# Optimization experiments

Measured on AMD Instinct MI355X. Metric: run time of the kernel, lower is better.

The kernel has to match this reference:

```python
import jax, jax.numpy as jnp
import numpy as np

N = 50000          # nodes
E = 1600000        # edges
IN_C = 128
HID = 128
OUT_C = 1
NUM_LAYERS = 3     # extra conv2 applications
NUM_GRAPHS = 128


def setup_inputs() -> dict:
    key = jax.random.key(0)
    ks = jax.random.split(key, 10)
    x = jax.random.normal(ks[0], (N, IN_C), dtype=jnp.float32)
    edge_index = jax.random.randint(ks[1], (2, E), 0, N, dtype=jnp.int64)
    batch = jnp.sort(jax.random.randint(ks[2], (N,), 0, NUM_GRAPHS, dtype=jnp.int64))
    s1 = 1.0 / np.sqrt(IN_C)
    s2 = 1.0 / np.sqrt(HID)
    W1 = jax.random.uniform(ks[3], (IN_C, HID), jnp.float32, -s1, s1)
    b1 = jnp.zeros((HID,), jnp.float32)
    W2 = jax.random.uniform(ks[4], (HID, HID), jnp.float32, -s2, s2)
    b2 = jnp.zeros((HID,), jnp.float32)
    Wfc = jax.random.uniform(ks[5], (HID, OUT_C), jnp.float32, -s2, s2)
    bfc = jnp.zeros((OUT_C,), jnp.float32)
    return {"x": x, "edge_index": edge_index, "batch": batch,
            "W1": W1, "b1": b1, "W2": W2, "b2": b2, "Wfc": Wfc, "bfc": bfc}


def _gcn_conv(x, W, b, src, dst, dinv):
    # GCNConv: h = X W; out[i] = sum_{j->i} h[j]/sqrt(d_j d_i) + h[i]/d_i + b
    # (self-loops added, symmetric degree normalization, deg includes self-loop)
    h = x @ W                                   # [N, out]
    coef = dinv[src] * dinv[dst]                # [E]
    agg = jax.ops.segment_sum(h[src] * coef[:, None], dst, num_segments=N)
    agg = agg + h * (dinv * dinv)[:, None]      # self-loop contribution
    return agg + b


def reference(x, edge_index, batch, W1, b1, W2, b2, Wfc, bfc):
    src, dst = edge_index[0], edge_index[1]
    # degree of target nodes, +1 for self-loop
    deg = jax.ops.segment_sum(jnp.ones((E,), x.dtype), dst, num_segments=N) + 1.0
    dinv = jax.lax.rsqrt(deg)

    h = jax.nn.relu(_gcn_conv(x, W1, b1, src, dst, dinv))
    for _ in range(NUM_LAYERS):
        h = jax.nn.relu(_gcn_conv(h, W2, b2, src, dst, dinv))
    # dropout is identity here (eval / deterministic reference)

    # global_mean_pool over graphs in the batch
    sums = jax.ops.segment_sum(h, batch, num_segments=NUM_GRAPHS)
    counts = jax.ops.segment_sum(jnp.ones((N,), h.dtype), batch, num_segments=NUM_GRAPHS)
    pooled = sums / jnp.clip(counts, 1.0)[:, None]   # [G, HID]
    return pooled @ Wfc + bfc                        # [G, OUT_C]
```

## Files before the change

### kernel.cpp

```cpp
#include <hip/hip_runtime.h>
#include <hip/hip_bf16.h>


__global__ void count_deg_kernel(const int* __restrict__ dst, int* __restrict__ deg, int E) {
    int i = blockIdx.x * blockDim.x + threadIdx.x;
    int e = i * 4;
    if (e + 3 < E) {
        int4 d = *(const int4*)(dst + e);
        atomicAdd(&deg[d.x], 1);
        atomicAdd(&deg[d.y], 1);
        atomicAdd(&deg[d.z], 1);
        atomicAdd(&deg[d.w], 1);
    } else {
        for (; e < E; e++) atomicAdd(&deg[dst[e]], 1);
    }
}

__global__ void dinv_kernel(const int* __restrict__ deg, float* __restrict__ dinv,
                            float* __restrict__ h0, float* __restrict__ h1,
                            int n, int ns) {
    int i = blockIdx.x * blockDim.x + threadIdx.x;
    if (i < n) dinv[i] = (float)(1.0 / sqrt((double)(deg[i] + 1)));
    if (i < 128) {
        int p = i >> 5, c = i & 31;
        size_t off = (size_t)p * ns * 32 + (size_t)n * 32 + c;
        h0[off] = 0.f;
        h1[off] = 0.f;
    }
}

__global__ void scan_blocksum_kernel(const int* __restrict__ cnt, int* __restrict__ bsum,
                                     int n2) {
    __shared__ int red[256];
    int t = threadIdx.x;
    int i = blockIdx.x * 256 + t;
    red[t] = (i < n2) ? cnt[i] : 0;
    __syncthreads();
    for (int off = 128; off > 0; off >>= 1) {
        if (t < off) red[t] += red[t + off];
        __syncthreads();
    }
    if (t == 0) bsum[blockIdx.x] = red[0];
}

__global__ __launch_bounds__(1024) void scan_bsum_kernel(const int* __restrict__ bsum,
                                                         int* __restrict__ boff, int nb) {
    __shared__ int s[1024];
    int t = threadIdx.x;
    int v = (t < nb) ? bsum[t] : 0;
    s[t] = v;
    __syncthreads();
    for (int off = 1; off < 1024; off <<= 1) {
        int u = (t >= off) ? s[t - off] : 0;
        __syncthreads();
        s[t] += u;
        __syncthreads();
    }
    if (t < nb) boff[t] = s[t] - v;
}

__global__ void scan_final_kernel(const int* __restrict__ cnt, const int* __restrict__ boff,
                                  int* __restrict__ row, int n2) {
    __shared__ int s[256];
    int t = threadIdx.x;
    int b = blockIdx.x;
    int i = b * 256 + t;
    int v = (i < n2) ? cnt[i] : 0;
    s[t] = v;
    __syncthreads();
    for (int off = 1; off < 256; off <<= 1) {
        int u = (t >= off) ? s[t - off] : 0;
        __syncthreads();
        s[t] += u;
        __syncthreads();
    }
    int incl = s[t];
    int base = boff[b];
    if (i < n2) row[i] = base + incl - v;
    if (i == n2 - 1) row[n2] = base + incl;
}

__global__ __launch_bounds__(256) void csr_fill_kernel(const int* __restrict__ src,
                                                       const int* __restrict__ dst,
                                                       const int* __restrict__ row,
                                                       int* __restrict__ fill,
                                                       unsigned short* __restrict__ csr,
                                                       int E, int N) {
    int g  = blockIdx.x & 7;
    int gb = blockIdx.x >> 3;
    int group_blocks = gridDim.x >> 3;
    int R  = (N + 7) >> 3;
    int lo = g * R;
    int hi = lo + R; if (hi > N) hi = N;

    int tig    = gb * blockDim.x + threadIdx.x;
    int stride = group_blocks * blockDim.x;
    int nq = (E + 3) >> 2;

    for (int q = tig; q < nq; q += stride) {
        int e = q * 4;
        if (e + 3 < E) {
            int4 d = *(const int4*)(dst + e);
            if (d.x >= lo && d.x < hi) {
                int pos = row[d.x] + atomicAdd(&fill[d.x], 1);
                csr[pos] = (unsigned short)src[e + 0];
            }
            if (d.y >= lo && d.y < hi) {
                int pos = row[d.y] + atomicAdd(&fill[d.y], 1);
                csr[pos] = (unsigned short)src[e + 1];
            }
            if (d.z >= lo && d.z < hi) {
                int pos = row[d.z] + atomicAdd(&fill[d.z], 1);
                csr[pos] = (unsigned short)src[e + 2];
            }
            if (d.w >= lo && d.w < hi) {
                int pos = row[d.w] + atomicAdd(&fill[d.w], 1);
                csr[pos] = (unsigned short)src[e + 3];
            }
        } else {
            for (; e < E; e++) {
                int d = dst[e];
                if (d >= lo && d < hi) {
                    int pos = row[d] + atomicAdd(&fill[d], 1);
                    csr[pos] = (unsigned short)src[e];
                }
            }
        }
    }
}

__global__ __launch_bounds__(256) void gemm_kernel(const float* __restrict__ A,
                                                   const float* __restrict__ W,
                                                   const float* __restrict__ dinv,
                                                   float* __restrict__ C, int n, int ns,
                                                   int a_blocked) {
    __shared__ float sW[128 * 32];
    __shared__ float sA[2][128 * 16];
    int t = threadIdx.x;
    int col0 = (blockIdx.x & 3) * 32;
    int row0 = (blockIdx.x >> 2) * 128;

    #pragma unroll
    for (int i = 0; i < 4; i++) {
        int fidx = t + 256 * i;
        int k  = fidx >> 3;
        int c4 = fidx & 7;
        *(float4*)(sW + k * 32 + c4 * 4) =
            *(const float4*)(W + (size_t)k * 128 + col0 + c4 * 4);
    }

    auto a_src = [&](int f, int kb) -> const float* {
        int rowi = f >> 2;
        int q    = f & 3;
        int rr = row0 + rowi; if (rr > n - 1) rr = n - 1;
        return a_blocked
            ? (A + ((size_t)(kb >> 1) * ns + rr) * 32 + (kb & 1) * 16 + q * 4)
            : (A + (size_t)rr * 128 + kb * 16 + q * 4);
    };

    {
        float4 v0 = *(const float4*)a_src(t, 0);
        float4 v1 = *(const float4*)a_src(t + 256, 0);
        int f0 = t, f1 = t + 256;
        *(float4*)(&sA[0][(f0 >> 2) * 16 + (f0 & 3) * 4]) = v0;
        *(float4*)(&sA[1 - 1][(f1 >> 2) * 16 + (f1 & 3) * 4]) = v1;
    }
    __syncthreads();

    int cg = (t & 7) * 4;
    int g8 = (t >> 3);

    float acc[4][4];
    #pragma unroll
    for (int j = 0; j < 4; j++)
        #pragma unroll
        for (int c = 0; c < 4; c++) acc[j][c] = 0.f;

    #pragma unroll 1
    for (int kb = 0; kb < 8; kb++) {
        float4 pre0, pre1;
        if (kb < 7) {
            pre0 = *(const float4*)a_src(t, kb + 1);
            pre1 = *(const float4*)a_src(t + 256, kb + 1);
        }

        const float* wbase = sW + kb * 16 * 32 + cg;
        const float* abase = sA[kb & 1];
        #pragma unroll
        for (int kkq = 0; kkq < 4; kkq++) {
            float4 aq[4];
            #pragma unroll
            for (int j = 0; j < 4; j++)
                aq[j] = *(const float4*)(abase + (g8 + 32 * j) * 16 + kkq * 4);
            #pragma unroll
            for (int k2 = 0; k2 < 4; k2++) {
                float4 w = *(const float4*)(wbase + (kkq * 4 + k2) * 32);
                #pragma unroll
                for (int j = 0; j < 4; j++) {
                    float av = (k2 == 0) ? aq[j].x : (k2 == 1) ? aq[j].y
                             : (k2 == 2) ? aq[j].z : aq[j].w;
                    acc[j][0] = fmaf(av, w.x, acc[j][0]);
                    acc[j][1] = fmaf(av, w.y, acc[j][1]);
                    acc[j][2] = fmaf(av, w.z, acc[j][2]);
                    acc[j][3] = fmaf(av, w.w, acc[j][3]);
                }
            }
        }

        if (kb < 7) {
            float* nbuf = sA[(kb + 1) & 1];
            int f0 = t, f1 = t + 256;
            *(float4*)(&nbuf[(f0 >> 2) * 16 + (f0 & 3) * 4]) = pre0;
            *(float4*)(&nbuf[(f1 >> 2) * 16 + (f1 & 3) * 4]) = pre1;
        }
        __syncthreads();
    }

    int cb = col0 + cg;
    float* Cb = C + (size_t)(cb >> 5) * ns * 32 + (cb & 31);
    #pragma unroll
    for (int j = 0; j < 4; j++) {
        int rr = row0 + g8 + 32 * j;
        if (rr < n) {
            float dsc = dinv[rr];
            *(float4*)(Cb + (size_t)rr * 32) =
                make_float4(acc[j][0] * dsc, acc[j][1] * dsc,
                            acc[j][2] * dsc, acc[j][3] * dsc);
        }
    }
}

__global__ __launch_bounds__(256) void agg_kernel(const float* __restrict__ h,
                                                  const int* __restrict__ row_ptr,
                                                  const unsigned short* __restrict__ csr,
                                                  const float* __restrict__ dinv,
                                                  const float* __restrict__ bias,
                                                  float* __restrict__ out,
                                                  int n, int ns) {
    int p = blockIdx.x & 3;
    int i = (blockIdx.x >> 2) * 32 + (threadIdx.x >> 3);
    int q = threadIdx.x & 7;
    bool valid = (i < n);
    int iv = valid ? i : 0;

    const float* slice  = h   + (size_t)p * ns * 32;
    float*       oslice = out + (size_t)p * ns * 32;

    int beg = row_ptr[iv];
    int end = valid ? row_ptr[iv + 1] : beg;
    int qoff = q << 2;

    float di = dinv[iv];
    float4 self = *(const float4*)(slice + ((size_t)iv << 5) + qoff);
    float4 b4   = *(const float4*)(bias + p * 32 + qoff);

    float4 acc = make_float4(0.f, 0.f, 0.f, 0.f);

    int e = beg;
    int s0 = (int)__builtin_nontemporal_load(csr + e);
    int s1 = (int)__builtin_nontemporal_load(csr + e + 1);
    int s2 = (int)__builtin_nontemporal_load(csr + e + 2);
    int s3 = (int)__builtin_nontemporal_load(csr + e + 3);
    int s4 = (int)__builtin_nontemporal_load(csr + e + 4);
    int s5 = (int)__builtin_nontemporal_load(csr + e + 5);
    int s6 = (int)__builtin_nontemporal_load(csr + e + 6);
    int s7 = (int)__builtin_nontemporal_load(csr + e + 7);

    while (__any(e < end)) {
        int en = e + 8;
        int t0 = (int)__builtin_nontemporal_load(csr + en);
        int t1 = (int)__builtin_nontemporal_load(csr + en + 1);
        int t2 = (int)__builtin_nontemporal_load(csr + en + 2);
        int t3 = (int)__builtin_nontemporal_load(csr + en + 3);
        int t4 = (int)__builtin_nontemporal_load(csr + en + 4);
        int t5 = (int)__builtin_nontemporal_load(csr + en + 5);
        int t6 = (int)__builtin_nontemporal_load(csr + en + 6);
        int t7 = (int)__builtin_nontemporal_load(csr + en + 7);

        int g0 = (e     < end) ? s0 : n;
        int g1 = (e + 1 < end) ? s1 : n;
        int g2 = (e + 2 < end) ? s2 : n;
        int g3 = (e + 3 < end) ? s3 : n;
        int g4 = (e + 4 < end) ? s4 : n;
        int g5 = (e + 5 < end) ? s5 : n;
        int g6 = (e + 6 < end) ? s6 : n;
        int g7 = (e + 7 < end) ? s7 : n;

        float4 v0 = *(const float4*)(slice + ((size_t)g0 << 5) + qoff);
        float4 v1 = *(const float4*)(slice + ((size_t)g1 << 5) + qoff);
        float4 v2 = *(const float4*)(slice + ((size_t)g2 << 5) + qoff);
        float4 v3 = *(const float4*)(slice + ((size_t)g3 << 5) + qoff);
        float4 v4 = *(const float4*)(slice + ((size_t)g4 << 5) + qoff);
        float4 v5 = *(const float4*)(slice + ((size_t)g5 << 5) + qoff);
        float4 v6 = *(const float4*)(slice + ((size_t)g6 << 5) + qoff);
        float4 v7 = *(const float4*)(slice + ((size_t)g7 << 5) + qoff);

        acc.x += v0.x; acc.y += v0.y; acc.z += v0.z; acc.w += v0.w;
        acc.x += v1.x; acc.y += v1.y; acc.z += v1.z; acc.w += v1.w;
        acc.x += v2.x; acc.y += v2.y; acc.z += v2.z; acc.w += v2.w;
        acc.x += v3.x; acc.y += v3.y; acc.z += v3.z; acc.w += v3.w;
        acc.x += v4.x; acc.y += v4.y; acc.z += v4.z; acc.w += v4.w;
        acc.x += v5.x; acc.y += v5.y; acc.z += v5.z; acc.w += v5.w;
        acc.x += v6.x; acc.y += v6.y; acc.z += v6.z; acc.w += v6.w;
        acc.x += v7.x; acc.y += v7.y; acc.z += v7.z; acc.w += v7.w;

        e = en;
        s0 = t0; s1 = t1; s2 = t2; s3 = t3;
        s4 = t4; s5 = t5; s6 = t6; s7 = t7;
    }

    if (valid) {
        float4 o;
        o.x = fmaxf(fmaf(acc.x + self.x, di, b4.x), 0.f);
        o.y = fmaxf(fmaf(acc.y + self.y, di, b4.y), 0.f);
        o.z = fmaxf(fmaf(acc.z + self.z, di, b4.z), 0.f);
        o.w = fmaxf(fmaf(acc.w + self.w, di, b4.w), 0.f);
        *(float4*)(oslice + ((size_t)i << 5) + qoff) = o;
    }
}

__global__ __launch_bounds__(128) void pool_partial_kernel(const float* __restrict__ h,
                                                           const int* __restrict__ batch,
                                                           double* __restrict__ partials,
                                                           int n, int ns, int S) {
    int g = blockIdx.x / S;
    int s = blockIdx.x % S;
    int c = threadIdx.x;
    const float* hb = h + (size_t)(c >> 5) * ns * 32 + (c & 31);

    int lo = 0, hi = n;
    while (lo < hi) { int mid = (lo + hi) >> 1; if (batch[mid] < g) lo = mid + 1; else hi = mid; }
    int start = lo;
    lo = start; hi = n;
    while (lo < hi) { int mid = (lo + hi) >> 1; if (batch[mid] < g + 1) lo = mid + 1; else hi = mid; }
    int end = lo;

    int cnt = end - start;
    int per = (cnt + S - 1) / S;
    int rs = start + s * per;
    int re = rs + per; if (re > end) re = end;

    double a0 = 0.0, a1 = 0.0, a2 = 0.0, a3 = 0.0;
    int r = rs;
    for (; r + 4 <= re; r += 4) {
        a0 += (double)hb[(size_t)(r + 0) * 32];
        a1 += (double)hb[(size_t)(r + 1) * 32];
        a2 += (double)hb[(size_t)(r + 2) * 32];
        a3 += (double)hb[(size_t)(r + 3) * 32];
    }
    for (; r < re; r++) a0 += (double)hb[(size_t)r * 32];
    partials[(size_t)(g * S + s) * 128 + c] = (a0 + a1) + (a2 + a3);
}

__global__ __launch_bounds__(128) void pool_fc_final_kernel(const double* __restrict__ partials,
                                                            const int* __restrict__ batch,
                                                            const float* __restrict__ Wfc,
                                                            const float* __restrict__ bfc,
                                                            float* __restrict__ out,
                                                            int n, int S) {
    int g = blockIdx.x;
    int c = threadIdx.x;

    int lo = 0, hi = n;
    while (lo < hi) { int mid = (lo + hi) >> 1; if (batch[mid] < g) lo = mid + 1; else hi = mid; }
    int start = lo;
    lo = start; hi = n;
    while (lo < hi) { int mid = (lo + hi) >> 1; if (batch[mid] < g + 1) lo = mid + 1; else hi = mid; }
    int cnt = lo - start;

    double sum = 0.0;
    for (int s = 0; s < S; s++) sum += partials[(size_t)(g * S + s) * 128 + c];
    double mean = sum / (double)(cnt > 0 ? cnt : 1);
    double v = mean * (double)Wfc[c];

    __shared__ double red[128];
    red[c] = v;
    __syncthreads();
    for (int off = 64; off > 0; off >>= 1) {
        if (c < off) red[c] += red[c + off];
        __syncthreads();
    }
    if (c == 0) out[g] = (float)(red[0] + (double)bfc[0]);
}

extern "C" void kernel_launch(void* const* d_in, const int* in_sizes, int n_in,
                              void* d_out, int out_size, void* d_ws, size_t ws_size,
                              hipStream_t stream) {
    const float* x          = (const float*)d_in[0];
    const int*   edge_index = (const int*)d_in[1];
    const int*   batch      = (const int*)d_in[2];
    const float* W1  = (const float*)d_in[3];
    const float* b1  = (const float*)d_in[4];
    const float* W2  = (const float*)d_in[5];
    const float* b2  = (const float*)d_in[6];
    const float* Wfc = (const float*)d_in[7];
    const float* bfc = (const float*)d_in[8];
    float* out = (float*)d_out;

    const int N = in_sizes[2];
    const int E = in_sizes[1] / 2;
    const int G = out_size;
    const int NS = N + 1;

    const int* e_src = edge_index;
    const int* e_dst = edge_index + E;

    char* p = (char*)d_ws;
    auto alloc = [&](size_t bytes) {
        void* r = (void*)p;
        p += (bytes + 255) & ~(size_t)255;
        return r;
    };
    const int S = 8;
    const int NB = (N + 255) / 256;
    float*          h0        = (float*)alloc((size_t)NS * 128 * 4);
    float*          h1        = (float*)alloc((size_t)NS * 128 * 4);
    unsigned short* csr       = (unsigned short*)alloc(((size_t)E + 1024) * 2);
    int*            row       = (int*)  alloc((size_t)(N + 1) * 4);
    int*            deg       = (int*)  alloc((size_t)N * 4);
    int*            fill      = (int*)  alloc((size_t)N * 4);
    int*            bsum      = (int*)  alloc((size_t)NB * 4);
    int*            boff      = (int*)  alloc((size_t)NB * 4);
    float*          dinv      = (float*)alloc((size_t)N * 4);
    double*         partials  = (double*)alloc((size_t)G * S * 128 * 8);
    (void)ws_size; (void)n_in;

    hipMemsetAsync(deg,  0, (size_t)N * 4, stream);
    hipMemsetAsync(fill, 0, (size_t)N * 4, stream);

    int tb = 256;
    int e4 = (E + 3) / 4;
    count_deg_kernel<<<(e4 + tb - 1) / tb, tb, 0, stream>>>(e_dst, deg, E);
    dinv_kernel<<<(N + tb - 1) / tb, tb, 0, stream>>>(deg, dinv, h0, h1, N, NS);
    scan_blocksum_kernel<<<NB, 256, 0, stream>>>(deg, bsum, N);
    scan_bsum_kernel<<<1, 1024, 0, stream>>>(bsum, boff, NB);
    scan_final_kernel<<<NB, 256, 0, stream>>>(deg, boff, row, N);
    csr_fill_kernel<<<1024, tb, 0, stream>>>(e_src, e_dst, row, fill, csr, E, N);

    int gemm_blocks = 4 * ((N + 127) / 128);
    int agg_blocks  = 4 * ((N + 31) / 32);

    gemm_kernel<<<gemm_blocks, 256, 0, stream>>>(x, W1, dinv, h1, N, NS, 0);
    agg_kernel<<<agg_blocks, 256, 0, stream>>>(h1, row, csr, dinv, b1, h0, N, NS);

    for (int l = 0; l < 3; l++) {
        gemm_kernel<<<gemm_blocks, 256, 0, stream>>>(h0, W2, dinv, h1, N, NS, 1);
        agg_kernel<<<agg_blocks, 256, 0, stream>>>(h1, row, csr, dinv, b2, h0, N, NS);
    }

    pool_partial_kernel<<<G * S, 128, 0, stream>>>(h0, batch, partials, N, NS, S);
    pool_fc_final_kernel<<<G, 128, 0, stream>>>(partials, batch, Wfc, bfc, out, N, S);
}
```

Measured before the change: 710.1 us.

## Retile GEMM to 64 rows by all 128 columns with streamed weight tiles

```diff
diff --git a/kernel.cpp b/kernel.cpp
--- a/kernel.cpp
+++ b/kernel.cpp
@@ -134,98 +134,101 @@
                                                    const float* __restrict__ dinv,
                                                    float* __restrict__ C, int n, int ns,
                                                    int a_blocked) {
-    __shared__ float sW[128 * 32];
-    __shared__ float sA[2][128 * 16];
+    __shared__ float sW[2][16 * 128];
+    __shared__ float sA[2][16 * 68];
     int t = threadIdx.x;
-    int col0 = (blockIdx.x & 3) * 32;
-    int row0 = (blockIdx.x >> 2) * 128;
-
-    #pragma unroll
-    for (int i = 0; i < 4; i++) {
-        int fidx = t + 256 * i;
-        int k  = fidx >> 3;
-        int c4 = fidx & 7;
-        *(float4*)(sW + k * 32 + c4 * 4) =
-            *(const float4*)(W + (size_t)k * 128 + col0 + c4 * 4);
-    }
-
-    auto a_src = [&](int f, int kb) -> const float* {
-        int rowi = f >> 2;
-        int q    = f & 3;
-        int rr = row0 + rowi; if (rr > n - 1) rr = n - 1;
+    int row0 = blockIdx.x * 64;
+
+    int a_rowi = t >> 2;
+    int a_q    = t & 3;
+    int w_krow = t >> 4;
+    int w_c    = (t & 15) * 8;
+
+    auto a_src = [&](int kb) -> const float* {
+        int rr = row0 + a_rowi; if (rr > n - 1) rr = n - 1;
         return a_blocked
-            ? (A + ((size_t)(kb >> 1) * ns + rr) * 32 + (kb & 1) * 16 + q * 4)
-            : (A + (size_t)rr * 128 + kb * 16 + q * 4);
+            ? (A + ((size_t)(kb >> 1) * ns + rr) * 32 + (kb & 1) * 16 + a_q * 4)
+            : (A + (size_t)rr * 128 + kb * 16 + a_q * 4);
     };
 
     {
-        float4 v0 = *(const float4*)a_src(t, 0);
-        float4 v1 = *(const float4*)a_src(t + 256, 0);
-        int f0 = t, f1 = t + 256;
-        *(float4*)(&sA[0][(f0 >> 2) * 16 + (f0 & 3) * 4]) = v0;
-        *(float4*)(&sA[1 - 1][(f1 >> 2) * 16 + (f1 & 3) * 4]) = v1;
+        float4 av = *(const float4*)a_src(0);
+        float4 w0 = *(const float4*)(W + (size_t)w_krow * 128 + w_c);
+        float4 w1 = *(const float4*)(W + (size_t)w_krow * 128 + w_c + 4);
+        sA[0][(a_q * 4 + 0) * 68 + a_rowi] = av.x;
+        sA[0][(a_q * 4 + 1) * 68 + a_rowi] = av.y;
+        sA[0][(a_q * 4 + 2) * 68 + a_rowi] = av.z;
+        sA[0][(a_q * 4 + 3) * 68 + a_rowi] = av.w;
+        *(float4*)(&sW[0][w_krow * 128 + w_c])     = w0;
+        *(float4*)(&sW[0][w_krow * 128 + w_c + 4]) = w1;
     }
     __syncthreads();
 
-    int cg = (t & 7) * 4;
-    int g8 = (t >> 3);
-
-    float acc[4][4];
+    int rg = t >> 4;
+    int cg = (t & 15) * 8;
+
+    float acc[4][8];
     #pragma unroll
     for (int j = 0; j < 4; j++)
         #pragma unroll
-        for (int c = 0; c < 4; c++) acc[j][c] = 0.f;
+        for (int c = 0; c < 8; c++) acc[j][c] = 0.f;
 
     #pragma unroll 1
     for (int kb = 0; kb < 8; kb++) {
-        float4 pre0, pre1;
+        float4 pa, pw0, pw1;
         if (kb < 7) {
-            pre0 = *(const float4*)a_src(t, kb + 1);
-            pre1 = *(const float4*)a_src(t + 256, kb + 1);
+            pa  = *(const float4*)a_src(kb + 1);
+            pw0 = *(const float4*)(W + (size_t)((kb + 1) * 16 + w_krow) * 128 + w_c);
+            pw1 = *(const float4*)(W + (size_t)((kb + 1) * 16 + w_krow) * 128 + w_c + 4);
         }
 
-        const float* wbase = sW + kb * 16 * 32 + cg;
-        const float* abase = sA[kb & 1];
+        const float* ab = sA[kb & 1];
+        const float* wb = sW[kb & 1];
         #pragma unroll
-        for (int kkq = 0; kkq < 4; kkq++) {
-            float4 aq[4];
+        for (int k = 0; k < 16; k++) {
+            float4 a4 = *(const float4*)(ab + k * 68 + rg * 4);
+            float4 w0 = *(const float4*)(wb + k * 128 + cg);
+            float4 w1 = *(const float4*)(wb + k * 128 + cg + 4);
             #pragma unroll
-            for (int j = 0; j < 4; j++)
-                aq[j] = *(const float4*)(abase + (g8 + 32 * j) * 16 + kkq * 4);
-            #pragma unroll
-            for (int k2 = 0; k2 < 4; k2++) {
-                float4 w = *(const float4*)(wbase + (kkq * 4 + k2) * 32);
-                #pragma unroll
-                for (int j = 0; j < 4; j++) {
-                    float av = (k2 == 0) ? aq[j].x : (k2 == 1) ? aq[j].y
-                             : (k2 == 2) ? aq[j].z : aq[j].w;
-                    acc[j][0] = fmaf(av, w.x, acc[j][0]);
-                    acc[j][1] = fmaf(av, w.y, acc[j][1]);
-                    acc[j][2] = fmaf(av, w.z, acc[j][2]);
-                    acc[j][3] = fmaf(av, w.w, acc[j][3]);
-                }
+            for (int j = 0; j < 4; j++) {
+                float av = (j == 0) ? a4.x : (j == 1) ? a4.y : (j == 2) ? a4.z : a4.w;
+                acc[j][0] = fmaf(av, w0.x, acc[j][0]);
+                acc[j][1] = fmaf(av, w0.y, acc[j][1]);
+                acc[j][2] = fmaf(av, w0.z, acc[j][2]);
+                acc[j][3] = fmaf(av, w0.w, acc[j][3]);
+                acc[j][4] = fmaf(av, w1.x, acc[j][4]);
+                acc[j][5] = fmaf(av, w1.y, acc[j][5]);
+                acc[j][6] = fmaf(av, w1.z, acc[j][6]);
+                acc[j][7] = fmaf(av, w1.w, acc[j][7]);
             }
         }
 
         if (kb < 7) {
-            float* nbuf = sA[(kb + 1) & 1];
-            int f0 = t, f1 = t + 256;
-            *(float4*)(&nbuf[(f0 >> 2) * 16 + (f0 & 3) * 4]) = pre0;
-            *(float4*)(&nbuf[(f1 >> 2) * 16 + (f1 & 3) * 4]) = pre1;
+            int nb = (kb + 1) & 1;
+            sA[nb][(a_q * 4 + 0) * 68 + a_rowi] = pa.x;
+            sA[nb][(a_q * 4 + 1) * 68 + a_rowi] = pa.y;
+            sA[nb][(a_q * 4 + 2) * 68 + a_rowi] = pa.z;
+            sA[nb][(a_q * 4 + 3) * 68 + a_rowi] = pa.w;
+            *(float4*)(&sW[nb][w_krow * 128 + w_c])     = pw0;
+            *(float4*)(&sW[nb][w_krow * 128 + w_c + 4]) = pw1;
         }
         __syncthreads();
     }
 
-    int cb = col0 + cg;
-    float* Cb = C + (size_t)(cb >> 5) * ns * 32 + (cb & 31);
+    int p  = cg >> 5;
+    int cw = cg & 31;
+    float* Cb = C + (size_t)p * ns * 32 + cw;
     #pragma unroll
     for (int j = 0; j < 4; j++) {
-        int rr = row0 + g8 + 32 * j;
+        int rr = row0 + rg * 4 + j;
         if (rr < n) {
             float dsc = dinv[rr];
             *(float4*)(Cb + (size_t)rr * 32) =
                 make_float4(acc[j][0] * dsc, acc[j][1] * dsc,
                             acc[j][2] * dsc, acc[j][3] * dsc);
+            *(float4*)(Cb + (size_t)rr * 32 + 4) =
+                make_float4(acc[j][4] * dsc, acc[j][5] * dsc,
+                            acc[j][6] * dsc, acc[j][7] * dsc);
         }
     }
 }
@@ -437,7 +440,7 @@
     scan_final_kernel<<<NB, 256, 0, stream>>>(deg, boff, row, N);
     csr_fill_kernel<<<1024, tb, 0, stream>>>(e_src, e_dst, row, fill, csr, E, N);
 
-    int gemm_blocks = 4 * ((N + 127) / 128);
+    int gemm_blocks = (N + 63) / 64;
     int agg_blocks  = 4 * ((N + 31) / 32);
 
     gemm_kernel<<<gemm_blocks, 256, 0, stream>>>(x, W1, dinv, h1, N, NS, 0);
```

After: 711.0 us. No clear change (+0.1%).
